# Performance work log

Hardware: AMD Instinct MI355X
Metric: run time of the kernel (lower is better)

Reference implementation:

```python
import jax, jax.numpy as jnp
import numpy as np

BSZ, SEQ, HID = 8, 4096, 1024
N_EXPERTS = 8
CAPACITY = 512  # expert_capacity_per_batch; effective cap = min(SEQ, CAPACITY)
SCALE = 1.0     # routed_scaling_factor


def setup_inputs() -> dict:
    key = jax.random.key(0)
    k1, k2 = jax.random.split(key)
    hidden_states = jax.random.normal(k1, (BSZ, SEQ, HID), dtype=jnp.float32)
    # kaiming_uniform_(a=sqrt(5)) on [d,e] -> bound = 1/sqrt(fan_in=d)
    bound = 1.0 / np.sqrt(HID)
    weight = jax.random.uniform(k2, (HID, N_EXPERTS), dtype=jnp.float32,
                                minval=-bound, maxval=bound)
    return {"hidden_states": hidden_states, "weight": weight}


def reference(hidden_states, weight):
    bsz, seq_len, h = hidden_states.shape
    # gating logits in fp32: [b, s, e]
    logits = jnp.einsum('bsd,de->bse', hidden_states.astype(jnp.float32),
                        weight.astype(jnp.float32))
    affinity = jax.nn.softmax(logits, axis=-1)          # [b, s, e]
    affinity = jnp.transpose(affinity, (0, 2, 1))       # [b, e, s]
    cap = min(seq_len, CAPACITY)                        # static
    # Each expert picks its top-`cap` tokens (sorted descending, like torch.topk)
    topk_scores, topk_indices = jax.lax.top_k(affinity, cap)  # [b, e, cap]
    topk_scores = topk_scores * SCALE
    # dense dispatch mask [b, e, cap, s]: one-hot over token positions
    dispatch_mask = jax.nn.one_hot(topk_indices, seq_len, dtype=jnp.float32)
    return topk_indices, topk_scores, dispatch_mask
```

## Files before the change

### kernel.cpp

```cpp
#include <hip/hip_runtime.h>

constexpr int BSZ = 8, SEQ = 4096, HID = 1024, NE = 8, CAP = 512;
constexpr int ROWS = BSZ * NE;
constexpr size_t IDX_ELEMS = (size_t)ROWS * CAP;
constexpr size_t SCR_OFF = IDX_ELEMS;
constexpr size_t MASK_OFF = IDX_ELEMS * 2;
constexpr size_t MASK_ELEMS = (size_t)ROWS * CAP * SEQ;
constexpr size_t AFF_ELEMS = (size_t)ROWS * SEQ;

__global__ __launch_bounds__(128) void gating_zero_kernel(const float* __restrict__ hidden,
                                                          const float* __restrict__ weight,
                                                          float* __restrict__ aff,
                                                          float* __restrict__ out,
                                                          long long zero_elems)
{
    __shared__ float hls[16][68];
    __shared__ float wls[8][68];
    __shared__ float lls[16][8];

    const int tid = threadIdx.x;
    const int T0 = blockIdx.x * 16;
    const int t = tid >> 3;
    const int e = tid & 7;

    float v0 = 0.f, v1 = 0.f, v2 = 0.f, v3 = 0.f;
    for (int c = 0; c < 16; ++c) {
        __syncthreads();
#pragma unroll
        for (int k = 0; k < 2; ++k) {
            const int j = tid + k * 128;
            const int tt = j >> 4, q = j & 15;
            const float4 v = *(const float4*)(hidden + (size_t)(T0 + tt) * HID + c * 64 + 4 * q);
            *(float4*)&hls[tt][4 * q] = v;
        }
#pragma unroll
        for (int k = 0; k < 4; ++k) {
            const int j = tid + k * 128;
            const int dd = j >> 3, ee = j & 7;
            wls[ee][dd] = weight[(size_t)(c * 64 + dd) * NE + ee];
        }
        __syncthreads();
#pragma unroll
        for (int k = 0; k < 4; ++k) {
            const int base = 16 * k;
            const float4 hA = *(const float4*)&hls[t][base + 0];
            const float4 hB = *(const float4*)&hls[t][base + 4];
            const float4 hC = *(const float4*)&hls[t][base + 8];
            const float4 hD = *(const float4*)&hls[t][base + 12];
            const float4 wA = *(const float4*)&wls[e][base + 0];
            const float4 wB = *(const float4*)&wls[e][base + 4];
            const float4 wC = *(const float4*)&wls[e][base + 8];
            const float4 wD = *(const float4*)&wls[e][base + 12];
            v0 = __fadd_rn(__fmul_rn(hA.x, wA.x),
                 __fadd_rn(__fmul_rn(hB.x, wB.x),
                 __fadd_rn(__fmul_rn(hC.x, wC.x),
                 __fadd_rn(__fmul_rn(hD.x, wD.x), v0))));
            v1 = __fadd_rn(__fmul_rn(hA.y, wA.y),
                 __fadd_rn(__fmul_rn(hB.y, wB.y),
                 __fadd_rn(__fmul_rn(hC.y, wC.y),
                 __fadd_rn(__fmul_rn(hD.y, wD.y), v1))));
            v2 = __fadd_rn(__fmul_rn(hA.z, wA.z),
                 __fadd_rn(__fmul_rn(hB.z, wB.z),
                 __fadd_rn(__fmul_rn(hC.z, wC.z),
                 __fadd_rn(__fmul_rn(hD.z, wD.z), v2))));
            v3 = __fadd_rn(__fmul_rn(hA.w, wA.w),
                 __fadd_rn(__fmul_rn(hB.w, wB.w),
                 __fadd_rn(__fmul_rn(hC.w, wC.w),
                 __fadd_rn(__fmul_rn(hD.w, wD.w), v3))));
        }
    }
    const float logit = __fadd_rn(__fadd_rn(v0, v1), __fadd_rn(v2, v3));

    lls[t][e] = logit;
    __syncthreads();

    float l[8];
#pragma unroll
    for (int k = 0; k < 8; ++k) l[k] = lls[t][k];
    float m = l[0];
#pragma unroll
    for (int k = 1; k < 8; ++k) m = fmaxf(m, l[k]);
    float p[8];
#pragma unroll
    for (int k = 0; k < 8; ++k)
        p[k] = (float)exp((double)__fsub_rn(l[k], m));
    const float s = __fadd_rn(__fadd_rn(__fadd_rn(p[0], p[1]), __fadd_rn(p[2], p[3])),
                              __fadd_rn(__fadd_rn(p[4], p[5]), __fadd_rn(p[6], p[7])));
    const float a = __fdiv_rn(p[e], s);

    const int token = T0 + t;
    const int b = token >> 12;
    const int sidx = token & (SEQ - 1);
    aff[((size_t)b * NE + e) * SEQ + sidx] = a;

    const long long nz4 = zero_elems >> 2;
    float4* mz = (float4*)(out + MASK_OFF);
    const float4 z4 = make_float4(0.f, 0.f, 0.f, 0.f);
    const long long stride = (long long)gridDim.x * 128;
    for (long long i = (long long)blockIdx.x * 128 + tid; i < nz4; i += stride)
        mz[i] = z4;
}

__global__ __launch_bounds__(1024) void sort_kernel(const float* __restrict__ aff,
                                                    float* __restrict__ out)
{
    __shared__ unsigned long long keys[SEQ];
    const int row = blockIdx.x;
    const float* a = aff + (size_t)row * SEQ;
    for (int i = threadIdx.x; i < SEQ; i += 1024) {
        const unsigned int fb = __float_as_uint(a[i]);
        keys[i] = ((unsigned long long)fb << 32) | (unsigned int)(SEQ - 1 - i);
    }
    for (int len = 2; len <= SEQ; len <<= 1) {
        for (int stride = len >> 1; stride > 0; stride >>= 1) {
            __syncthreads();
            for (int t = threadIdx.x; t < SEQ / 2; t += 1024) {
                const int i = (t << 1) - (t & (stride - 1));
                const int j = i + stride;
                const unsigned long long ki = keys[i], kj = keys[j];
                const bool desc = ((i & len) == 0);
                if (desc ? (ki < kj) : (ki > kj)) { keys[i] = kj; keys[j] = ki; }
            }
        }
    }
    __syncthreads();
    if (threadIdx.x < CAP) {
        const int t = threadIdx.x;
        const unsigned long long k = keys[t];
        const int idx = (SEQ - 1) - (int)(unsigned int)(k & 0xffffffffu);
        out[(size_t)row * CAP + t] = (float)idx;
        out[SCR_OFF + (size_t)row * CAP + t] =
            __uint_as_float((unsigned int)(k >> 32));
    }
}

__global__ void tailzero_kernel(float* __restrict__ out)
{
    const long long n4 = (long long)(AFF_ELEMS >> 2);
    float4* mz = (float4*)(out + MASK_OFF + MASK_ELEMS - AFF_ELEMS);
    const long long i = (long long)blockIdx.x * blockDim.x + threadIdx.x;
    if (i < n4) mz[i] = make_float4(0.f, 0.f, 0.f, 0.f);
}

__global__ void scatter_kernel(float* __restrict__ out)
{
    const int p = blockIdx.x * blockDim.x + threadIdx.x;
    if (p < (int)IDX_ELEMS) {
        const int idx = (int)out[p];
        out[MASK_OFF + (size_t)p * SEQ + idx] = 1.0f;
    }
}

extern "C" void kernel_launch(void* const* d_in, const int* in_sizes, int n_in,
                              void* d_out, int out_size, void* d_ws, size_t ws_size,
                              hipStream_t stream)
{
    const float* hidden = (const float*)d_in[0];
    const float* weight = (const float*)d_in[1];
    float* out = (float*)d_out;

    const bool use_ws = (ws_size >= AFF_ELEMS * sizeof(float));
    float* aff = use_ws ? (float*)d_ws
                        : (out + MASK_OFF + MASK_ELEMS - AFF_ELEMS);

    const long long zero_elems = use_ws ? (long long)MASK_ELEMS
                                        : (long long)(MASK_ELEMS - AFF_ELEMS);

    gating_zero_kernel<<<2048, 128, 0, stream>>>(hidden, weight, aff, out, zero_elems);
    sort_kernel<<<ROWS, 1024, 0, stream>>>(aff, out);
    if (!use_ws)
        tailzero_kernel<<<256, 256, 0, stream>>>(out);
    scatter_kernel<<<(int)((IDX_ELEMS + 255) / 256), 256, 0, stream>>>(out);
}
```

Before: 699.7 us.

## Split mask zeroing across gating and sort kernels to overlap with sort

Mask zero-fill no longer runs inside the gating blocks. It is split into two pieces handled by extra blocks appended to each grid: the first 9/16 of the mask is zeroed by dedicated blocks in the gating launch, and the rest by extra blocks in the sort launch. The sort launch has only 64 working blocks, so most CUs sit idle there; this move is meant to fill them with memory-bound zeroing and hide the zero-fill bandwidth cost behind the sort. The risk is that the zero blocks in the sort grid compete for HBM or delay scheduling of the sort blocks, and the split ratio is a tuning constant.

```diff
diff --git a/kernel.cpp b/kernel.cpp
--- a/kernel.cpp
+++ b/kernel.cpp
@@ -7,13 +7,29 @@
 constexpr size_t MASK_OFF = IDX_ELEMS * 2;
 constexpr size_t MASK_ELEMS = (size_t)ROWS * CAP * SEQ;
 constexpr size_t AFF_ELEMS = (size_t)ROWS * SEQ;
+constexpr size_t ZA_ELEMS = MASK_ELEMS * 9 / 16;
 
-__global__ __launch_bounds__(128) void gating_zero_kernel(const float* __restrict__ hidden,
-                                                          const float* __restrict__ weight,
-                                                          float* __restrict__ aff,
-                                                          float* __restrict__ out,
-                                                          long long zero_elems)
+constexpr int GATE_BLOCKS = 2048;
+constexpr int ZERO1_BLOCKS = 1024;
+constexpr int SORT_BLOCKS = ROWS;
+constexpr int ZERO2_BLOCKS = 192;
+
+__global__ __launch_bounds__(128) void gate_zeroA_kernel(const float* __restrict__ hidden,
+                                                         const float* __restrict__ weight,
+                                                         float* __restrict__ aff,
+                                                         float* __restrict__ out)
 {
+    if (blockIdx.x >= (unsigned)GATE_BLOCKS) {
+        const long long nz4 = (long long)(ZA_ELEMS >> 2);
+        float4* mz = (float4*)(out + MASK_OFF);
+        const float4 z4 = make_float4(0.f, 0.f, 0.f, 0.f);
+        const long long stride = (long long)ZERO1_BLOCKS * 128;
+        for (long long i = (long long)(blockIdx.x - GATE_BLOCKS) * 128 + threadIdx.x;
+             i < nz4; i += stride)
+            mz[i] = z4;
+        return;
+    }
+
     __shared__ float hls[16][68];
     __shared__ float wls[8][68];
     __shared__ float lls[16][8];
@@ -92,18 +108,24 @@
     const int b = token >> 12;
     const int sidx = token & (SEQ - 1);
     aff[((size_t)b * NE + e) * SEQ + sidx] = a;
-
-    const long long nz4 = zero_elems >> 2;
-    float4* mz = (float4*)(out + MASK_OFF);
-    const float4 z4 = make_float4(0.f, 0.f, 0.f, 0.f);
-    const long long stride = (long long)gridDim.x * 128;
-    for (long long i = (long long)blockIdx.x * 128 + tid; i < nz4; i += stride)
-        mz[i] = z4;
 }
 
-__global__ __launch_bounds__(1024) void sort_kernel(const float* __restrict__ aff,
-                                                    float* __restrict__ out)
+__global__ __launch_bounds__(1024) void sort_zeroB_kernel(const float* __restrict__ aff,
+                                                          float* __restrict__ out,
+                                                          long long zend_elems)
 {
+    if (blockIdx.x >= (unsigned)SORT_BLOCKS) {
+        const long long z0 = (long long)(ZA_ELEMS >> 2);
+        const long long nz4 = zend_elems >> 2;
+        float4* mz = (float4*)(out + MASK_OFF);
+        const float4 z4 = make_float4(0.f, 0.f, 0.f, 0.f);
+        const long long stride = (long long)ZERO2_BLOCKS * 1024;
+        for (long long i = z0 + (long long)(blockIdx.x - SORT_BLOCKS) * 1024 + threadIdx.x;
+             i < nz4; i += stride)
+            mz[i] = z4;
+        return;
+    }
+
     __shared__ unsigned long long keys[SEQ];
     const int row = blockIdx.x;
     const float* a = aff + (size_t)row * SEQ;
@@ -163,11 +185,11 @@
     float* aff = use_ws ? (float*)d_ws
                         : (out + MASK_OFF + MASK_ELEMS - AFF_ELEMS);
 
-    const long long zero_elems = use_ws ? (long long)MASK_ELEMS
-                                        : (long long)(MASK_ELEMS - AFF_ELEMS);
+    const long long zend = use_ws ? (long long)MASK_ELEMS
+                                  : (long long)(MASK_ELEMS - AFF_ELEMS);
 
-    gating_zero_kernel<<<2048, 128, 0, stream>>>(hidden, weight, aff, out, zero_elems);
-    sort_kernel<<<ROWS, 1024, 0, stream>>>(aff, out);
+    gate_zeroA_kernel<<<GATE_BLOCKS + ZERO1_BLOCKS, 128, 0, stream>>>(hidden, weight, aff, out);
+    sort_zeroB_kernel<<<SORT_BLOCKS + ZERO2_BLOCKS, 1024, 0, stream>>>(aff, out, zend);
     if (!use_ws)
         tailzero_kernel<<<256, 256, 0, stream>>>(out);
     scatter_kernel<<<(int)((IDX_ELEMS + 255) / 256), 256, 0, stream>>>(out);
```

Result: faster. 652.7 us (-6.7%).
